# Kernel optimization log

Hardware: AMD Instinct MI355X
Metric: run time of the kernel (lower is better)

## Reference

```python
import jax, jax.numpy as jnp
import numpy as np


def _chamfer(xyz1, xyz2):
    # xyz1: [B,N,3], xyz2: [B,M,3]
    sq1 = jnp.sum(xyz1 * xyz1, axis=-1)               # [B,N]
    sq2 = jnp.sum(xyz2 * xyz2, axis=-1)               # [B,M]
    cross = jnp.einsum('bnc,bmc->bnm', xyz1, xyz2)    # [B,N,M]
    d = sq1[:, :, None] + sq2[:, None, :] - 2.0 * cross  # [B,N,M] squared dists
    dist1 = jnp.min(d, axis=2)                        # [B,N]
    idx1 = jnp.argmin(d, axis=2).astype(jnp.int32)    # [B,N]
    dist2 = jnp.min(d, axis=1)                        # [B,M]
    idx2 = jnp.argmin(d, axis=1).astype(jnp.int32)    # [B,M]
    return dist1, dist2, idx1, idx2


def setup_inputs() -> dict:
    key = jax.random.key(0)
    k1, k2 = jax.random.split(key)
    B, N, M = 2, 8192, 8192
    xyz1 = jax.random.normal(k1, (B, N, 3), dtype=jnp.float32)
    xyz2 = jax.random.normal(k2, (B, M, 3), dtype=jnp.float32)
    return {"xyz1": xyz1, "xyz2": xyz2}


def reference(xyz1, xyz2):
    # Matches ChamferDistanceFunction.forward: returns (dist1, dist2, idx1, idx2)
    # with SQUARED distances, as in the CUDA kernel.
    return _chamfer(xyz1, xyz2)
```

## Files before the change

### kernel.cpp

```cpp
#include <hip/hip_runtime.h>
#include <stdint.h>

#define TPB   256
#define Q     4
#define CHUNK 512

typedef unsigned long long ull;

__device__ __forceinline__ uint32_t enc_f32(float f) {
    uint32_t u = __float_as_uint(f);
    return (u & 0x80000000u) ? ~u : (u | 0x80000000u);
}

__device__ __forceinline__ float sq_np(float x, float y, float z) {
    return __fadd_rn(__fadd_rn(__fmul_rn(x, x), __fmul_rn(y, y)), __fmul_rn(z, z));
}

__global__ void __launch_bounds__(TPB) chamfer_pass1(
    const float* __restrict__ xyz1, const float* __restrict__ xyz2,
    ull* __restrict__ P, int B, int N, int M)
{
    __shared__ float4 pts[CHUNK];

    int z   = blockIdx.z;
    int dir = z / B;
    int b   = z - dir * B;

    const float* src; const float* dst; int Ns, Nd; size_t ebase;
    if (dir == 0) { src = xyz1; dst = xyz2; Ns = N; Nd = M; ebase = (size_t)b * N; }
    else          { src = xyz2; dst = xyz1; Ns = M; Nd = N; ebase = (size_t)B * N + (size_t)b * M; }

    int t     = threadIdx.x;
    int mbase = blockIdx.y * CHUNK;

    for (int i = t; i < CHUNK; i += TPB) {
        int m = mbase + i;
        if (m < Nd) {
            const float* p = dst + ((size_t)b * Nd + m) * 3;
            float x = p[0], y = p[1], zz = p[2];
            pts[i] = make_float4(x, y, zz, sq_np(x, y, zz));
        } else {
            pts[i] = make_float4(0.f, 0.f, 0.f, 3.0e38f);
        }
    }

    int n0 = blockIdx.x * (TPB * Q) + t;
    float qx[Q], qy[Q], qz[Q], qs[Q];
    #pragma unroll
    for (int k = 0; k < Q; ++k) {
        int n = n0 + k * TPB;
        if (n < Ns) {
            const float* p = src + ((size_t)b * Ns + n) * 3;
            qx[k] = p[0]; qy[k] = p[1]; qz[k] = p[2];
            qs[k] = sq_np(qx[k], qy[k], qz[k]);
        } else {
            qx[k] = 0.f; qy[k] = 0.f; qz[k] = 0.f; qs[k] = 0.f;
        }
    }
    __syncthreads();

    float best[Q];
    int   bidx[Q];
    #pragma unroll
    for (int k = 0; k < Q; ++k) { best[k] = 3.4e38f; bidx[k] = 0; }

    #pragma unroll 4
    for (int i = 0; i < CHUNK; ++i) {
        float4 q = pts[i];
        #pragma unroll
        for (int k = 0; k < Q; ++k) {
            float cross = __fadd_rn(__fadd_rn(__fmul_rn(qx[k], q.x), __fmul_rn(qy[k], q.y)),
                                    __fmul_rn(qz[k], q.z));
            float s = __fadd_rn(qs[k], q.w);
            float d = fmaf(-2.0f, cross, s);
            if (d < best[k]) { best[k] = d; bidx[k] = mbase + i; }
        }
    }

    #pragma unroll
    for (int k = 0; k < Q; ++k) {
        int n = n0 + k * TPB;
        if (n < Ns) {
            ull packed = ((ull)enc_f32(best[k]) << 32) | (unsigned int)bidx[k];
            atomicMin(&P[ebase + n], packed);
        }
    }
}

__global__ void __launch_bounds__(256) chamfer_unpack(
    const ull* __restrict__ P, float* __restrict__ out, int entries)
{
    int e = blockIdx.x * 256 + threadIdx.x;
    if (e < entries) {
        ull pk = P[e];
        uint32_t encu = (uint32_t)(pk >> 32);
        uint32_t idx  = (uint32_t)pk;
        uint32_t bits = (encu & 0x80000000u) ? (encu & 0x7FFFFFFFu) : ~encu;
        out[e]           = __uint_as_float(bits);
        out[entries + e] = (float)idx;
    }
}

__global__ void __launch_bounds__(1024) chamfer_unpack_inplace(float* __restrict__ out)
{
    const int entries = 32768;
    const ull* P = (const ull*)out;
    int t = threadIdx.x;
    ull v[32];
    #pragma unroll
    for (int k = 0; k < 32; ++k) v[k] = P[t + k * 1024];
    __syncthreads();
    #pragma unroll
    for (int k = 0; k < 32; ++k) {
        int e = t + k * 1024;
        ull pk = v[k];
        uint32_t encu = (uint32_t)(pk >> 32);
        uint32_t idx  = (uint32_t)pk;
        uint32_t bits = (encu & 0x80000000u) ? (encu & 0x7FFFFFFFu) : ~encu;
        out[e]           = __uint_as_float(bits);
        out[entries + e] = (float)idx;
    }
}

extern "C" void kernel_launch(void* const* d_in, const int* in_sizes, int n_in,
                              void* d_out, int out_size, void* d_ws, size_t ws_size,
                              hipStream_t stream) {
    const float* xyz1 = (const float*)d_in[0];
    const float* xyz2 = (const float*)d_in[1];
    const int B = 2;
    const int N = in_sizes[0] / (B * 3);
    const int M = in_sizes[1] / (B * 3);

    float* out = (float*)d_out;
    const int entries = B * N + B * M;
    const size_t pbytes = (size_t)entries * sizeof(ull);

    int maxP = (N > M) ? N : M;
    dim3 grid((maxP + TPB * Q - 1) / (TPB * Q), (maxP + CHUNK - 1) / CHUNK, 2 * B);

    if (ws_size >= pbytes) {
        ull* P = (ull*)d_ws;
        hipMemsetAsync(d_ws, 0xFF, pbytes, stream);
        chamfer_pass1<<<grid, TPB, 0, stream>>>(xyz1, xyz2, P, B, N, M);
        chamfer_unpack<<<(entries + 255) / 256, 256, 0, stream>>>(P, out, entries);
    } else {
        ull* P = (ull*)d_out;
        hipMemsetAsync(d_out, 0xFF, pbytes, stream);
        chamfer_pass1<<<grid, TPB, 0, stream>>>(xyz1, xyz2, P, B, N, M);
        if (entries == 32768) {
            chamfer_unpack_inplace<<<1, 1024, 0, stream>>>(out);
        } else {
            chamfer_unpack<<<1, 1, 0, stream>>>((const ull*)d_out, out, 0);
        }
    }
}
```

Baseline: 121.0 us.

## Vectorize distance loop with packed float2 math and per-chunk partial reduction

Stores the target points in structure-of-arrays shared memory and computes two distances at a time with float2 vector ops, which may map to packed FP32 instructions. Distance and index are packed into a 64-bit key so each candidate needs one unsigned compare instead of a compare plus select. The raw float bits are used without sign encoding, which relies on distances being non-negative. When the workspace is large enough, each chunk writes its own partial results and a separate reduce kernel combines them, replacing the memset and global atomics. CHUNK shrinks to 128, giving more blocks but more partial slices to reduce.

```diff
diff --git a/kernel.cpp b/kernel.cpp
--- a/kernel.cpp
+++ b/kernel.cpp
@@ -3,24 +3,22 @@
 
 #define TPB   256
 #define Q     4
-#define CHUNK 512
+#define CHUNK 128
 
 typedef unsigned long long ull;
-
-__device__ __forceinline__ uint32_t enc_f32(float f) {
-    uint32_t u = __float_as_uint(f);
-    return (u & 0x80000000u) ? ~u : (u | 0x80000000u);
-}
+typedef float v2f __attribute__((ext_vector_type(2)));
 
 __device__ __forceinline__ float sq_np(float x, float y, float z) {
     return __fadd_rn(__fadd_rn(__fmul_rn(x, x), __fmul_rn(y, y)), __fmul_rn(z, z));
 }
 
+template<int MODE>
 __global__ void __launch_bounds__(TPB) chamfer_pass1(
     const float* __restrict__ xyz1, const float* __restrict__ xyz2,
-    ull* __restrict__ P, int B, int N, int M)
+    ull* __restrict__ P, int B, int N, int M, int entriesTot)
 {
-    __shared__ float4 pts[CHUNK];
+#pragma clang fp contract(off)
+    __shared__ float sx[CHUNK], sy[CHUNK], sz[CHUNK], ss[CHUNK];
 
     int z   = blockIdx.z;
     int dir = z / B;
@@ -33,14 +31,14 @@
     int t     = threadIdx.x;
     int mbase = blockIdx.y * CHUNK;
 
-    for (int i = t; i < CHUNK; i += TPB) {
-        int m = mbase + i;
+    if (t < CHUNK) {
+        int m = mbase + t;
         if (m < Nd) {
             const float* p = dst + ((size_t)b * Nd + m) * 3;
             float x = p[0], y = p[1], zz = p[2];
-            pts[i] = make_float4(x, y, zz, sq_np(x, y, zz));
+            sx[t] = x; sy[t] = y; sz[t] = zz; ss[t] = sq_np(x, y, zz);
         } else {
-            pts[i] = make_float4(0.f, 0.f, 0.f, 3.0e38f);
+            sx[t] = 0.f; sy[t] = 0.f; sz[t] = 0.f; ss[t] = 3.0e38f;
         }
     }
 
@@ -53,27 +51,40 @@
             const float* p = src + ((size_t)b * Ns + n) * 3;
             qx[k] = p[0]; qy[k] = p[1]; qz[k] = p[2];
             qs[k] = sq_np(qx[k], qy[k], qz[k]);
-        } else {
-            qx[k] = 0.f; qy[k] = 0.f; qz[k] = 0.f; qs[k] = 0.f;
-        }
+        } else { qx[k] = 0.f; qy[k] = 0.f; qz[k] = 0.f; qs[k] = 0.f; }
     }
     __syncthreads();
 
-    float best[Q];
-    int   bidx[Q];
+    ull best[Q];
     #pragma unroll
-    for (int k = 0; k < Q; ++k) { best[k] = 3.4e38f; bidx[k] = 0; }
+    for (int k = 0; k < Q; ++k) best[k] = ~0ull;
 
+    const v2f n2 = {-2.0f, -2.0f};
     #pragma unroll 4
-    for (int i = 0; i < CHUNK; ++i) {
-        float4 q = pts[i];
+    for (int i = 0; i < CHUNK; i += 4) {
+        float4 x4 = *(const float4*)&sx[i];
+        float4 y4 = *(const float4*)&sy[i];
+        float4 z4 = *(const float4*)&sz[i];
+        float4 s4 = *(const float4*)&ss[i];
+        v2f xA = {x4.x, x4.y}, xB = {x4.z, x4.w};
+        v2f yA = {y4.x, y4.y}, yB = {y4.z, y4.w};
+        v2f zA = {z4.x, z4.y}, zB = {z4.z, z4.w};
+        v2f sA = {s4.x, s4.y}, sB = {s4.z, s4.w};
+        unsigned i0 = (unsigned)(mbase + i);
+
         #pragma unroll
         for (int k = 0; k < Q; ++k) {
-            float cross = __fadd_rn(__fadd_rn(__fmul_rn(qx[k], q.x), __fmul_rn(qy[k], q.y)),
-                                    __fmul_rn(qz[k], q.z));
-            float s = __fadd_rn(qs[k], q.w);
-            float d = fmaf(-2.0f, cross, s);
-            if (d < best[k]) { best[k] = d; bidx[k] = mbase + i; }
+            v2f qxx = {qx[k], qx[k]}, qyy = {qy[k], qy[k]};
+            v2f qzz = {qz[k], qz[k]}, qss = {qs[k], qs[k]};
+            v2f crA = (qxx * xA + qyy * yA) + qzz * zA;
+            v2f crB = (qxx * xB + qyy * yB) + qzz * zB;
+            v2f dA  = __builtin_elementwise_fma(n2, crA, qss + sA);
+            v2f dB  = __builtin_elementwise_fma(n2, crB, qss + sB);
+            ull p;
+            p = ((ull)__float_as_uint(dA.x) << 32) | (i0 + 0u); if (p < best[k]) best[k] = p;
+            p = ((ull)__float_as_uint(dA.y) << 32) | (i0 + 1u); if (p < best[k]) best[k] = p;
+            p = ((ull)__float_as_uint(dB.x) << 32) | (i0 + 2u); if (p < best[k]) best[k] = p;
+            p = ((ull)__float_as_uint(dB.y) << 32) | (i0 + 3u); if (p < best[k]) best[k] = p;
         }
     }
 
@@ -81,24 +92,34 @@
     for (int k = 0; k < Q; ++k) {
         int n = n0 + k * TPB;
         if (n < Ns) {
-            ull packed = ((ull)enc_f32(best[k]) << 32) | (unsigned int)bidx[k];
-            atomicMin(&P[ebase + n], packed);
+            if (MODE == 0) P[(size_t)blockIdx.y * entriesTot + ebase + n] = best[k];
+            else           atomicMin(&P[ebase + n], best[k]);
         }
     }
+}
+
+__global__ void __launch_bounds__(256) chamfer_reduce(
+    const ull* __restrict__ P, float* __restrict__ out, int entries, int nch)
+{
+    int e = blockIdx.x * 256 + threadIdx.x;
+    if (e >= entries) return;
+    ull best = ~0ull;
+    for (int c = 0; c < nch; ++c) {
+        ull v = P[(size_t)c * entries + e];
+        if (v < best) best = v;
+    }
+    out[e]           = __uint_as_float((uint32_t)(best >> 32));
+    out[entries + e] = (float)(uint32_t)best;
 }
 
 __global__ void __launch_bounds__(256) chamfer_unpack(
     const ull* __restrict__ P, float* __restrict__ out, int entries)
 {
     int e = blockIdx.x * 256 + threadIdx.x;
-    if (e < entries) {
-        ull pk = P[e];
-        uint32_t encu = (uint32_t)(pk >> 32);
-        uint32_t idx  = (uint32_t)pk;
-        uint32_t bits = (encu & 0x80000000u) ? (encu & 0x7FFFFFFFu) : ~encu;
-        out[e]           = __uint_as_float(bits);
-        out[entries + e] = (float)idx;
-    }
+    if (e >= entries) return;
+    ull pk = P[e];
+    out[e]           = __uint_as_float((uint32_t)(pk >> 32));
+    out[entries + e] = (float)(uint32_t)pk;
 }
 
 __global__ void __launch_bounds__(1024) chamfer_unpack_inplace(float* __restrict__ out)
@@ -114,11 +135,8 @@
     for (int k = 0; k < 32; ++k) {
         int e = t + k * 1024;
         ull pk = v[k];
-        uint32_t encu = (uint32_t)(pk >> 32);
-        uint32_t idx  = (uint32_t)pk;
-        uint32_t bits = (encu & 0x80000000u) ? (encu & 0x7FFFFFFFu) : ~encu;
-        out[e]           = __uint_as_float(bits);
-        out[entries + e] = (float)idx;
+        out[e]           = __uint_as_float((uint32_t)(pk >> 32));
+        out[entries + e] = (float)(uint32_t)pk;
     }
 }
 
@@ -133,24 +151,26 @@
 
     float* out = (float*)d_out;
     const int entries = B * N + B * M;
-    const size_t pbytes = (size_t)entries * sizeof(ull);
+    const int maxP = (N > M) ? N : M;
+    const int nych = (maxP + CHUNK - 1) / CHUNK;
+    dim3 grid((maxP + TPB * Q - 1) / (TPB * Q), nych, 2 * B);
 
-    int maxP = (N > M) ? N : M;
-    dim3 grid((maxP + TPB * Q - 1) / (TPB * Q), (maxP + CHUNK - 1) / CHUNK, 2 * B);
+    const size_t partBytes = (size_t)nych * entries * sizeof(ull);
+    const size_t pBytes    = (size_t)entries * sizeof(ull);
 
-    if (ws_size >= pbytes) {
+    if (ws_size >= partBytes) {
         ull* P = (ull*)d_ws;
-        hipMemsetAsync(d_ws, 0xFF, pbytes, stream);
-        chamfer_pass1<<<grid, TPB, 0, stream>>>(xyz1, xyz2, P, B, N, M);
+        chamfer_pass1<0><<<grid, TPB, 0, stream>>>(xyz1, xyz2, P, B, N, M, entries);
+        chamfer_reduce<<<(entries + 255) / 256, 256, 0, stream>>>(P, out, entries, nych);
+    } else if (ws_size >= pBytes) {
+        ull* P = (ull*)d_ws;
+        hipMemsetAsync(d_ws, 0xFF, pBytes, stream);
+        chamfer_pass1<1><<<grid, TPB, 0, stream>>>(xyz1, xyz2, P, B, N, M, entries);
         chamfer_unpack<<<(entries + 255) / 256, 256, 0, stream>>>(P, out, entries);
     } else {
         ull* P = (ull*)d_out;
-        hipMemsetAsync(d_out, 0xFF, pbytes, stream);
-        chamfer_pass1<<<grid, TPB, 0, stream>>>(xyz1, xyz2, P, B, N, M);
-        if (entries == 32768) {
-            chamfer_unpack_inplace<<<1, 1024, 0, stream>>>(out);
-        } else {
-            chamfer_unpack<<<1, 1, 0, stream>>>((const ull*)d_out, out, 0);
-        }
+        hipMemsetAsync(d_out, 0xFF, pBytes, stream);
+        chamfer_pass1<1><<<grid, TPB, 0, stream>>>(xyz1, xyz2, P, B, N, M, entries);
+        chamfer_unpack_inplace<<<1, 1024, 0, stream>>>(out);
     }
 }
```

New measurement: 145.6 us. 20.3% more time.
